# Kernel tuning notes

Hardware: AMD Instinct MI355X
Metric: run time of the kernel (lower is better)

## Reference

```python
import jax, jax.numpy as jnp
import numpy as np

SCALE = 1.0 / np.sqrt(512.0).astype(np.float32)  # attention() hardcodes d_k=512


def setup_inputs() -> dict:
    key = jax.random.key(0)
    ks = jax.random.split(key, 9)
    B, S, D = 4, 2048, 512
    mk = lambda k, shape: jax.random.normal(k, shape, dtype=jnp.float32) * 0.05
    return {
        "q": mk(ks[0], (B, S, D)),
        "k": mk(ks[1], (B, S, D)),
        "v": mk(ks[2], (B, S, D)),
        "WQ_w": mk(ks[3], (D, D)),
        "WQ_b": mk(ks[4], (D,)),
        "WK_w": mk(ks[5], (D, D)),
        "WK_b": mk(ks[6], (D,)),
        "WV_w": mk(ks[7], (D, D)),
        "WV_b": mk(ks[8], (D,)),
    }


def reference(q, k, v, WQ_w, WQ_b, WK_w, WK_b, WV_w, WV_b):
    # torch nn.Linear: y = x @ W.T + b
    qp = q @ WQ_w.T + WQ_b  # [B,S,dk]
    kp = k @ WK_w.T + WK_b  # [B,S,dk]
    vp = v @ WV_w.T + WV_b  # [B,S,dv]
    qk = jnp.einsum("bqd,bkd->bqk", qp, kp) * SCALE  # [B,Sq,Sk]
    S = qk.shape[1]
    tril = jnp.tril(jnp.ones((S, S), dtype=qk.dtype))  # multiplicative causal mask
    qk = qk * tril
    # NOTE: original applies softmax over dim=1 (the query axis), faithfully kept.
    attn = jax.nn.softmax(qk, axis=1)
    out = jnp.einsum("bqk,bkd->bqd", attn, vp)  # [B,Sq,dv]
    return out
```

## Files before the change

kernel.cpp:

```cpp
#include <hip/hip_runtime.h>
#include <hip/hip_bf16.h>


#define S_LEN 2048
#define D_DIM 512
#define SCALE_F 0.044194173824159216f

typedef __attribute__((ext_vector_type(8))) short s8v;
typedef __attribute__((ext_vector_type(4))) short s4v;
typedef __attribute__((ext_vector_type(4))) float f4v;

enum { EPI_BIAS = 0, EPI_BIAS_T = 1, EPI_SCORES = 2 };

#define SBAR()    __builtin_amdgcn_s_barrier()
#define SCHEDB()  __builtin_amdgcn_sched_barrier(0)
#define WAITV(n)  asm volatile("s_waitcnt vmcnt(" #n ")")
#define WAITL0()  asm volatile("s_waitcnt lgkmcnt(0)")

__device__ __forceinline__ short f2bf_s(float f) {
  union { __hip_bfloat16 b; short s; } u; u.b = __float2bfloat16(f); return u.s;
}
__device__ __forceinline__ float bf2f_s(short h) {
  union { short s; __hip_bfloat16 b; } u; u.s = h; return __bfloat162float(u.b);
}

__device__ __forceinline__ void glds16(const short* g, short* l) {
  __builtin_amdgcn_global_load_lds((const __attribute__((address_space(1))) void*)g,
                                   (__attribute__((address_space(3))) void*)l, 16, 0, 0);
}

__device__ __forceinline__ unsigned lds_addr(const short* p) {
  return (unsigned)(unsigned long long)(const __attribute__((address_space(3))) short*)p;
}

__device__ __forceinline__ s8v dsr128(unsigned a) {
  s8v r;
  asm volatile("ds_read_b128 %0, %1" : "=&v"(r) : "v"(a));
  return r;
}

template <int EPI>
__device__ __forceinline__ void gemm_core(
    const short* __restrict__ A, const short* __restrict__ B,
    short* __restrict__ C, const float* __restrict__ bias,
    short* SMEM, int N, int K, size_t sCz, int m0, int n0, int bz,
    float* __restrict__ Z)
{
  const int tid  = threadIdx.x;
  const int w    = tid >> 6;
  const int lane = tid & 63;
  const int quad = lane >> 4;
  const int l16  = lane & 15;
  const int wm   = (w >> 1) * 64;
  const int wn   = (w & 1) * 64;

  const int strow = tid >> 3;
  const int gl = ((tid & 7) ^ (strow & 7)) * 8;

  f4v acc[4][4];
#pragma unroll
  for (int i = 0; i < 4; ++i)
#pragma unroll
    for (int j = 0; j < 4; ++j)
#pragma unroll
      for (int r = 0; r < 4; ++r) acc[i][j][r] = 0.0f;

  const short* Ag = A + (size_t)(m0 + strow) * K + gl;
  const short* Bg = B + (size_t)(n0 + strow) * K + gl;
  const size_t pstr = (size_t)32 * K;
  const int t8 = tid * 8;
  const int swq = l16 & 7;

  const unsigned base = lds_addr(SMEM);
  unsigned aoff[4], boff[4];
#pragma unroll
  for (int ii = 0; ii < 4; ++ii)
    aoff[ii] = base + (unsigned)((wm + ii * 16 + l16) * 128 + ((quad ^ swq) * 16));
#pragma unroll
  for (int j = 0; j < 4; ++j)
    boff[j] = base + 16384u + (unsigned)((wn + j * 16 + l16) * 128 + ((quad ^ swq) * 16));

  const int niter = K >> 6;

#pragma unroll
  for (int p = 0; p < 4; ++p) glds16(Ag + p * pstr, SMEM + t8 + p * 2048);
#pragma unroll
  for (int p = 0; p < 4; ++p) glds16(Bg + p * pstr, SMEM + 8192 + t8 + p * 2048);

  for (int i = 0; i < niter; ++i) {
    const int c = i & 1;
    if (i + 1 < niter) {
      const int k1 = (i + 1) << 6;
      short* dA = SMEM + (1 - c) * 16384 + t8;
#pragma unroll
      for (int p = 0; p < 4; ++p) glds16(Ag + k1 + p * pstr, dA + p * 2048);
#pragma unroll
      for (int p = 0; p < 4; ++p) glds16(Bg + k1 + p * pstr, dA + 8192 + p * 2048);
      SCHEDB();
      WAITV(8);
    } else {
      WAITV(0);
    }
    SBAR();
    SCHEDB();

    const unsigned cofs = (unsigned)(c << 15);
#pragma unroll
    for (int kk = 0; kk < 2; ++kk) {
      const unsigned kx = (unsigned)(kk << 6);
      s8v af[4], bf[4];
#pragma unroll
      for (int ii = 0; ii < 4; ++ii) af[ii] = dsr128((aoff[ii] ^ kx) + cofs);
#pragma unroll
      for (int j = 0; j < 4; ++j)   bf[j]  = dsr128((boff[j] ^ kx) + cofs);
      WAITL0();
      SCHEDB();
      __builtin_amdgcn_s_setprio(1);
#pragma unroll
      for (int ii = 0; ii < 4; ++ii)
#pragma unroll
        for (int j = 0; j < 4; ++j)
          acc[ii][j] = __builtin_amdgcn_mfma_f32_16x16x32_bf16(af[ii], bf[j], acc[ii][j], 0, 0, 0);
      __builtin_amdgcn_s_setprio(0);
    }
    SBAR();
  }

  float bv[4];
  if (EPI == EPI_BIAS || EPI == EPI_BIAS_T) {
#pragma unroll
    for (int j = 0; j < 4; ++j) bv[j] = bias[n0 + wn + j * 16 + l16];
  }

  if (EPI == EPI_BIAS_T) {
#pragma unroll
    for (int i = 0; i < 4; ++i) {
#pragma unroll
      for (int j = 0; j < 4; ++j) {
        const int gn  = n0 + wn + j * 16 + l16;
        const int gmb = m0 + wm + i * 16 + quad * 4;
        const int bb = gmb >> 11, ssb = gmb & (S_LEN - 1);
        s4v o;
#pragma unroll
        for (int r = 0; r < 4; ++r) o[r] = f2bf_s(acc[i][j][r] + bv[j]);
        *(s4v*)&C[((size_t)bb * D_DIM + gn) * S_LEN + ssb] = o;
      }
    }
    return;
  }

  short* TB = SMEM;
  const int wbase = w * 2176;
  float csum[4] = {0.f, 0.f, 0.f, 0.f};

#pragma unroll
  for (int ph = 0; ph < 2; ++ph) {
    __syncthreads();
#pragma unroll
    for (int ii = 0; ii < 2; ++ii) {
      const int i = ph * 2 + ii;
#pragma unroll
      for (int j = 0; j < 4; ++j) {
        const int gn = n0 + wn + j * 16 + l16;
#pragma unroll
        for (int r = 0; r < 4; ++r) {
          short o;
          if (EPI == EPI_SCORES) {
            const int gm = m0 + wm + i * 16 + quad * 4 + r;
            const float f = (gm >= gn) ? (__expf(acc[i][j][r] * SCALE_F) - 1.0f) : 0.0f;
            csum[j] += f;
            o = f2bf_s(f);
          } else {
            o = f2bf_s(acc[i][j][r] + bv[j]);
          }
          TB[wbase + (ii * 16 + quad * 4 + r) * 68 + j * 16 + l16] = o;
        }
      }
    }
    __syncthreads();
#pragma unroll
    for (int p = 0; p < 4; ++p) {
      const int row = p * 8 + (lane >> 3);
      const int cg  = lane & 7;
      const s8v vv = *(const s8v*)&TB[wbase + row * 68 + cg * 8];
      const int gm = m0 + wm + ph * 32 + row;
      const int gn = n0 + wn + cg * 8;
      *(s8v*)&C[sCz + (size_t)gm * N + gn] = vv;
    }
  }

  if (EPI == EPI_SCORES) {
#pragma unroll
    for (int j = 0; j < 4; ++j) {
      float cs = csum[j];
      cs += __shfl_xor(cs, 16, 64);
      cs += __shfl_xor(cs, 32, 64);
      if (quad == 0) atomicAdd(&Z[(bz << 11) + n0 + wn + j * 16 + l16], cs);
    }
  }
}

__global__ __launch_bounds__(256, 2) void gemm_scoresF(
    const short* __restrict__ A, const short* __restrict__ B, short* __restrict__ C,
    float* __restrict__ Z)
{
  __shared__ __align__(16) short SMEM[32768];
  const int bid = blockIdx.x;
  const int bsw = (bid & 7) * 68 + (bid >> 3);
  const int bz  = bsw / 136;
  const int t   = bsw - bz * 136;
  int ti = (int)((sqrtf(8.0f * t + 1.0f) - 1.0f) * 0.5f);
  while ((ti + 1) * (ti + 2) / 2 <= t) ++ti;
  while (ti * (ti + 1) / 2 > t) --ti;
  const int tj = t - ti * (ti + 1) / 2;
  gemm_core<EPI_SCORES>(A + (size_t)bz * S_LEN * D_DIM, B + (size_t)bz * S_LEN * D_DIM,
                        C, nullptr, SMEM, S_LEN, D_DIM,
                        (size_t)bz * S_LEN * S_LEN, ti * 128, tj * 128, bz, Z);
}

__global__ __launch_bounds__(256, 2) void proj3(
    const short* __restrict__ a0, const short* __restrict__ a1, const short* __restrict__ a2,
    const short* __restrict__ b0, const short* __restrict__ b1, const short* __restrict__ b2,
    short* __restrict__ c0, short* __restrict__ c1, short* __restrict__ c2,
    const float* __restrict__ x0, const float* __restrict__ x1, const float* __restrict__ x2)
{
  __shared__ __align__(16) short SMEM[32768];
  const int bid = blockIdx.x;
  const int bsw = (bid & 7) * 96 + (bid >> 3);
  const int z   = bsw >> 8;
  const int rem = bsw & 255;
  const int m0  = (rem >> 2) * 128;
  const int n0  = (rem & 3) * 128;
  const short* A = (z == 0) ? a0 : (z == 1) ? a1 : a2;
  const short* B = (z == 0) ? b0 : (z == 1) ? b1 : b2;
  short*       C = (z == 0) ? c0 : (z == 1) ? c1 : c2;
  const float* bias = (z == 0) ? x0 : (z == 1) ? x1 : x2;
  if (z == 2)
    gemm_core<EPI_BIAS_T>(A, B, C, bias, SMEM, D_DIM, D_DIM, 0, m0, n0, 0, nullptr);
  else
    gemm_core<EPI_BIAS>(A, B, C, bias, SMEM, D_DIM, D_DIM, 0, m0, n0, 0, nullptr);
}

__global__ __launch_bounds__(256, 2) void gemm_outF(
    const short* __restrict__ F, const short* __restrict__ vpT,
    const float* __restrict__ Tv, float* __restrict__ out)
{
  __shared__ __align__(16) short SMEM[36864];

  const int tid  = threadIdx.x;
  const int h    = blockIdx.x;
  const int n0   = (h & 3) * 128;
  const int bz   = (h >> 2) & 3;
  const int zs   = h >> 4;
  const int mi   = (zs < 16) ? (31 - zs) : (zs - 16);
  const int m0   = mi * 64;

  const short* A = F   + (size_t)bz * S_LEN * S_LEN;
  const short* B = vpT + (size_t)bz * D_DIM * S_LEN;

  const int w    = tid >> 6;
  const int lane = tid & 63;
  const int quad = lane >> 4;
  const int l16  = lane & 15;
  const int wm   = (w >> 1) * 32;
  const int wn   = (w & 1) * 64;

  const int strow = tid >> 3;
  const int gl = ((tid & 7) ^ (strow & 7)) * 8;

  f4v acc[2][4];
#pragma unroll
  for (int i = 0; i < 2; ++i)
#pragma unroll
    for (int j = 0; j < 4; ++j)
#pragma unroll
      for (int r = 0; r < 4; ++r) acc[i][j][r] = 0.0f;

  const short* Ag = A + (size_t)(m0 + strow) * S_LEN + gl;
  const short* Bg = B + (size_t)(n0 + strow) * S_LEN + gl;
  const size_t pstr = (size_t)32 * S_LEN;
  const int t8 = tid * 8;
  const int swq = l16 & 7;

  const unsigned base = lds_addr(SMEM);
  unsigned aoff[2], boff[4];
#pragma unroll
  for (int ii = 0; ii < 2; ++ii)
    aoff[ii] = base + (unsigned)((wm + ii * 16 + l16) * 128 + ((quad ^ swq) * 16));
#pragma unroll
  for (int j = 0; j < 4; ++j)
    boff[j] = base + 8192u + (unsigned)((wn + j * 16 + l16) * 128 + ((quad ^ swq) * 16));

  const int niter = mi + 1;

#pragma unroll
  for (int pre = 0; pre < 2; ++pre) {
    short* dst = SMEM + pre * 12288 + t8;
    const int k0 = pre << 6;
#pragma unroll
    for (int p = 0; p < 2; ++p) glds16(Ag + k0 + p * pstr, dst + p * 2048);
#pragma unroll
    for (int p = 0; p < 4; ++p) glds16(Bg + k0 + p * pstr, dst + 4096 + p * 2048);
  }

  int cbuf = 0;
  for (int i = 0; i < niter; ++i) {
    if (i + 1 < niter) { WAITV(6); } else { WAITV(0); }
    SBAR();
    SCHEDB();

    if (i + 2 < niter) {
      int nb = cbuf + 2; if (nb >= 3) nb -= 3;
      const int k2 = (i + 2) << 6;
      short* dst = SMEM + nb * 12288 + t8;
#pragma unroll
      for (int p = 0; p < 2; ++p) glds16(Ag + k2 + p * pstr, dst + p * 2048);
#pragma unroll
      for (int p = 0; p < 4; ++p) glds16(Bg + k2 + p * pstr, dst + 4096 + p * 2048);
      SCHEDB();
    }

    const unsigned cofs = (unsigned)(cbuf * 24576);
    cbuf = (cbuf == 2) ? 0 : cbuf + 1;
#pragma unroll
    for (int kk = 0; kk < 2; ++kk) {
      const unsigned kx = (unsigned)(kk << 6);
      s8v af[2], bf[4];
#pragma unroll
      for (int ii = 0; ii < 2; ++ii) af[ii] = dsr128((aoff[ii] ^ kx) + cofs);
#pragma unroll
      for (int j = 0; j < 4; ++j)   bf[j]  = dsr128((boff[j] ^ kx) + cofs);
      WAITL0();
      SCHEDB();
      __builtin_amdgcn_s_setprio(1);
#pragma unroll
      for (int ii = 0; ii < 2; ++ii)
#pragma unroll
        for (int j = 0; j < 4; ++j)
          acc[ii][j] = __builtin_amdgcn_mfma_f32_16x16x32_bf16(af[ii], bf[j], acc[ii][j], 0, 0, 0);
      __builtin_amdgcn_s_setprio(0);
    }
  }

  float* Cf = out + (size_t)bz * S_LEN * D_DIM;
#pragma unroll
  for (int i = 0; i < 2; ++i) {
#pragma unroll
    for (int j = 0; j < 4; ++j) {
      const int gn = n0 + wn + j * 16 + l16;
      const float tvn = Tv[(bz << 9) + gn];
#pragma unroll
      for (int r = 0; r < 4; ++r) {
        const int gm = m0 + wm + i * 16 + quad * 4 + r;
        Cf[(size_t)gm * D_DIM + gn] = acc[i][j][r] + tvn;
      }
    }
  }
}

__global__ __launch_bounds__(256) void cvt_all(
    const float* __restrict__ q, const float* __restrict__ k, const float* __restrict__ v,
    const float* __restrict__ wq, const float* __restrict__ wk, const float* __restrict__ wv,
    short* __restrict__ qb, short* __restrict__ Wqb)
{
  const int y = blockIdx.y;
  const float* s; short* d; int i;
  if (blockIdx.x < 2048) {
    s = (y == 0) ? q : (y == 1) ? k : v;
    d = qb + (size_t)y * 4194304;
    i = (blockIdx.x * 256 + threadIdx.x) * 8;
  } else {
    s = (y == 0) ? wq : (y == 1) ? wk : wv;
    d = Wqb + (size_t)y * 262144;
    i = ((int)(blockIdx.x - 2048) * 256 + threadIdx.x) * 8;
  }
  const float4 f0 = *(const float4*)(s + i);
  const float4 f1 = *(const float4*)(s + i + 4);
  s8v o;
  o[0] = f2bf_s(f0.x); o[1] = f2bf_s(f0.y); o[2] = f2bf_s(f0.z); o[3] = f2bf_s(f0.w);
  o[4] = f2bf_s(f1.x); o[5] = f2bf_s(f1.y); o[6] = f2bf_s(f1.z); o[7] = f2bf_s(f1.w);
  *(s8v*)(d + i) = o;
}

__global__ __launch_bounds__(256) void scale_vpt_T(
    short* __restrict__ vpT, const float* __restrict__ ZF, float* __restrict__ Tv)
{
  __shared__ float red[4];
  const int b = blockIdx.y, d = blockIdx.x, tid = threadIdx.x;
  const size_t rowbase = ((size_t)(b * D_DIM + d)) * S_LEN;
  const float* zf = ZF + (b << 11);
  const int k0 = tid * 8;

  s8v v = *(s8v*)&vpT[rowbase + k0];
  float s = 0.0f;
#pragma unroll
  for (int i = 0; i < 8; ++i) {
    const float w = bf2f_s(v[i]) / (2048.0f + zf[k0 + i]);
    s += w;
    v[i] = f2bf_s(w);
  }
  *(s8v*)&vpT[rowbase + k0] = v;

#pragma unroll
  for (int off = 32; off >= 1; off >>= 1) s += __shfl_xor(s, off, 64);
  if ((tid & 63) == 0) red[tid >> 6] = s;
  __syncthreads();
  if (tid == 0) Tv[(b << 9) + d] = red[0] + red[1] + red[2] + red[3];
}

extern "C" void kernel_launch(void* const* d_in, const int* in_sizes, int n_in,
                              void* d_out, int out_size, void* d_ws, size_t ws_size,
                              hipStream_t stream) {
  const float* q   = (const float*)d_in[0];
  const float* k   = (const float*)d_in[1];
  const float* v   = (const float*)d_in[2];
  const float* WQw = (const float*)d_in[3];
  const float* WQb = (const float*)d_in[4];
  const float* WKw = (const float*)d_in[5];
  const float* WKb = (const float*)d_in[6];
  const float* WVw = (const float*)d_in[7];
  const float* WVb = (const float*)d_in[8];

  char* ws = (char*)d_ws;
  short* F   = (short*)(ws);
  short* qb  = (short*)(ws);
  short* Wqb = (short*)(ws + 25165824);
  short* qp  = (short*)(ws + 33554432);
  short* kp  = (short*)(ws + 41943040);
  short* vpT = (short*)(ws + 50331648);
  float* ZF  = (float*)(ws + 58720256);
  float* Tv  = (float*)(ws + 58753024);
  short* kb  = qb + 4194304;
  short* vb  = qb + 8388608;
  short* Wkb = Wqb + 262144;
  short* Wvb = Wqb + 524288;

  const dim3 blk(256);

  (void)hipMemsetAsync(ZF, 0, 4 * S_LEN * sizeof(float), stream);

  cvt_all<<<dim3(2176, 3), blk, 0, stream>>>(q, k, v, WQw, WKw, WVw, qb, Wqb);

  proj3<<<dim3(768), blk, 0, stream>>>(
      qb, kb, vb, Wqb, Wkb, Wvb, qp, kp, vpT, WQb, WKb, WVb);

  gemm_scoresF<<<dim3(544), blk, 0, stream>>>(qp, kp, F, ZF);

  scale_vpt_T<<<dim3(512, 4), blk, 0, stream>>>(vpT, ZF, Tv);

  gemm_outF<<<dim3(512), blk, 0, stream>>>(F, vpT, Tv, (float*)d_out);
}
```

Baseline: 168.5 us.

## Fuse V projection into scores kernel and fold memset into conversion

Splits the three-way projection kernel into a Q/K projection kernel and moves the V projection tiles into the scores kernel as extra blocks, so the V projection overlaps with the causal score GEMM's partially filled last wave. The bf16 copies of v and Wv now live in the output buffer, which is free until the final kernel. The separate memset of the column-sum buffer is replaced by zeroing inside the conversion kernel, removing one launch. This adds branching in a combined kernel and reuses the output buffer as scratch, which relies on that buffer not being read before the last kernel.

```diff
diff --git a/kernel.cpp b/kernel.cpp
--- a/kernel.cpp
+++ b/kernel.cpp
@@ -200,45 +200,52 @@
   }
 }
 
-__global__ __launch_bounds__(256, 2) void gemm_scoresF(
-    const short* __restrict__ A, const short* __restrict__ B, short* __restrict__ C,
-    float* __restrict__ Z)
+__global__ __launch_bounds__(256, 2) void proj_qk(
+    const short* __restrict__ a0, const short* __restrict__ a1,
+    const short* __restrict__ b0, const short* __restrict__ b1,
+    short* __restrict__ c0, short* __restrict__ c1,
+    const float* __restrict__ x0, const float* __restrict__ x1)
 {
   __shared__ __align__(16) short SMEM[32768];
   const int bid = blockIdx.x;
-  const int bsw = (bid & 7) * 68 + (bid >> 3);
-  const int bz  = bsw / 136;
-  const int t   = bsw - bz * 136;
-  int ti = (int)((sqrtf(8.0f * t + 1.0f) - 1.0f) * 0.5f);
-  while ((ti + 1) * (ti + 2) / 2 <= t) ++ti;
-  while (ti * (ti + 1) / 2 > t) --ti;
-  const int tj = t - ti * (ti + 1) / 2;
-  gemm_core<EPI_SCORES>(A + (size_t)bz * S_LEN * D_DIM, B + (size_t)bz * S_LEN * D_DIM,
-                        C, nullptr, SMEM, S_LEN, D_DIM,
-                        (size_t)bz * S_LEN * S_LEN, ti * 128, tj * 128, bz, Z);
-}
-
-__global__ __launch_bounds__(256, 2) void proj3(
-    const short* __restrict__ a0, const short* __restrict__ a1, const short* __restrict__ a2,
-    const short* __restrict__ b0, const short* __restrict__ b1, const short* __restrict__ b2,
-    short* __restrict__ c0, short* __restrict__ c1, short* __restrict__ c2,
-    const float* __restrict__ x0, const float* __restrict__ x1, const float* __restrict__ x2)
-{
-  __shared__ __align__(16) short SMEM[32768];
-  const int bid = blockIdx.x;
-  const int bsw = (bid & 7) * 96 + (bid >> 3);
+  const int bsw = (bid & 7) * 64 + (bid >> 3);
   const int z   = bsw >> 8;
   const int rem = bsw & 255;
   const int m0  = (rem >> 2) * 128;
   const int n0  = (rem & 3) * 128;
-  const short* A = (z == 0) ? a0 : (z == 1) ? a1 : a2;
-  const short* B = (z == 0) ? b0 : (z == 1) ? b1 : b2;
-  short*       C = (z == 0) ? c0 : (z == 1) ? c1 : c2;
-  const float* bias = (z == 0) ? x0 : (z == 1) ? x1 : x2;
-  if (z == 2)
-    gemm_core<EPI_BIAS_T>(A, B, C, bias, SMEM, D_DIM, D_DIM, 0, m0, n0, 0, nullptr);
-  else
-    gemm_core<EPI_BIAS>(A, B, C, bias, SMEM, D_DIM, D_DIM, 0, m0, n0, 0, nullptr);
+  const short* A = z ? a1 : a0;
+  const short* B = z ? b1 : b0;
+  short*       C = z ? c1 : c0;
+  const float* bias = z ? x1 : x0;
+  gemm_core<EPI_BIAS>(A, B, C, bias, SMEM, D_DIM, D_DIM, 0, m0, n0, 0, nullptr);
+}
+
+__global__ __launch_bounds__(256, 2) void scores_projv(
+    const short* __restrict__ qp, const short* __restrict__ kp, short* __restrict__ F,
+    float* __restrict__ Z,
+    const short* __restrict__ vb, const short* __restrict__ Wvb,
+    short* __restrict__ vpT, const float* __restrict__ xv)
+{
+  __shared__ __align__(16) short SMEM[32768];
+  const int bid = blockIdx.x;
+  if (bid < 544) {
+    const int bsw = (bid & 7) * 68 + (bid >> 3);
+    const int bz  = bsw / 136;
+    const int t   = bsw - bz * 136;
+    int ti = (int)((sqrtf(8.0f * t + 1.0f) - 1.0f) * 0.5f);
+    while ((ti + 1) * (ti + 2) / 2 <= t) ++ti;
+    while (ti * (ti + 1) / 2 > t) --ti;
+    const int tj = t - ti * (ti + 1) / 2;
+    gemm_core<EPI_SCORES>(qp + (size_t)bz * S_LEN * D_DIM, kp + (size_t)bz * S_LEN * D_DIM,
+                          F, nullptr, SMEM, S_LEN, D_DIM,
+                          (size_t)bz * S_LEN * S_LEN, ti * 128, tj * 128, bz, Z);
+  } else {
+    const int h   = bid - 544;
+    const int hsw = (h & 7) * 32 + (h >> 3);
+    const int m0  = (hsw >> 2) * 128;
+    const int n0  = (hsw & 3) * 128;
+    gemm_core<EPI_BIAS_T>(vb, Wvb, vpT, xv, SMEM, D_DIM, D_DIM, 0, m0, n0, 0, nullptr);
+  }
 }
 
 __global__ __launch_bounds__(256, 2) void gemm_outF(
@@ -361,17 +368,23 @@
 __global__ __launch_bounds__(256) void cvt_all(
     const float* __restrict__ q, const float* __restrict__ k, const float* __restrict__ v,
     const float* __restrict__ wq, const float* __restrict__ wk, const float* __restrict__ wv,
-    short* __restrict__ qb, short* __restrict__ Wqb)
+    short* __restrict__ qb, short* __restrict__ kb, short* __restrict__ vb,
+    short* __restrict__ Wqb, short* __restrict__ Wkb, short* __restrict__ Wvb,
+    float* __restrict__ ZF)
 {
   const int y = blockIdx.y;
   const float* s; short* d; int i;
   if (blockIdx.x < 2048) {
     s = (y == 0) ? q : (y == 1) ? k : v;
-    d = qb + (size_t)y * 4194304;
+    d = (y == 0) ? qb : (y == 1) ? kb : vb;
     i = (blockIdx.x * 256 + threadIdx.x) * 8;
+    if (y == 0) {
+      const int gid = blockIdx.x * 256 + threadIdx.x;
+      if (gid < 8192) ZF[gid] = 0.0f;
+    }
   } else {
     s = (y == 0) ? wq : (y == 1) ? wk : wv;
-    d = Wqb + (size_t)y * 262144;
+    d = (y == 0) ? Wqb : (y == 1) ? Wkb : Wvb;
     i = ((int)(blockIdx.x - 2048) * 256 + threadIdx.x) * 8;
   }
   const float4 f0 = *(const float4*)(s + i);
@@ -424,27 +437,25 @@
   char* ws = (char*)d_ws;
   short* F   = (short*)(ws);
   short* qb  = (short*)(ws);
+  short* kb  = qb + 4194304;
   short* Wqb = (short*)(ws + 25165824);
+  short* Wkb = Wqb + 262144;
   short* qp  = (short*)(ws + 33554432);
   short* kp  = (short*)(ws + 41943040);
   short* vpT = (short*)(ws + 50331648);
   float* ZF  = (float*)(ws + 58720256);
   float* Tv  = (float*)(ws + 58753024);
-  short* kb  = qb + 4194304;
-  short* vb  = qb + 8388608;
-  short* Wkb = Wqb + 262144;
-  short* Wvb = Wqb + 524288;
+  short* vb  = (short*)d_out;
+  short* Wvb = (short*)d_out + 4194304;
 
   const dim3 blk(256);
 
-  (void)hipMemsetAsync(ZF, 0, 4 * S_LEN * sizeof(float), stream);
-
-  cvt_all<<<dim3(2176, 3), blk, 0, stream>>>(q, k, v, WQw, WKw, WVw, qb, Wqb);
-
-  proj3<<<dim3(768), blk, 0, stream>>>(
-      qb, kb, vb, Wqb, Wkb, Wvb, qp, kp, vpT, WQb, WKb, WVb);
-
-  gemm_scoresF<<<dim3(544), blk, 0, stream>>>(qp, kp, F, ZF);
+  cvt_all<<<dim3(2176, 3), blk, 0, stream>>>(
+      q, k, v, WQw, WKw, WVw, qb, kb, vb, Wqb, Wkb, Wvb, ZF);
+
+  proj_qk<<<dim3(512), blk, 0, stream>>>(qb, kb, Wqb, Wkb, qp, kp, WQb, WKb);
+
+  scores_projv<<<dim3(800), blk, 0, stream>>>(qp, kp, F, ZF, vb, Wvb, vpT, WVb);
 
   scale_vpt_T<<<dim3(512, 4), blk, 0, stream>>>(vpT, ZF, Tv);
 
```

New measurement: 164.4 us. 1.02x faster.
